# Kernel optimization log

Measured on AMD Instinct MI355X. Metric: run time of the kernel, lower is better.

Reference implementation:

```python
import jax, jax.numpy as jnp
import numpy as np

B, T, D, H = 4, 2048, 1024, 16
HD = D // H  # 64


def setup_inputs() -> dict:
    key = jax.random.key(0)
    k1, k2, k3 = jax.random.split(key, 3)
    x = jax.random.normal(k1, (B, T, D), dtype=jnp.float32)
    # xavier-uniform-ish scaling for stability
    W_qkv = jax.random.normal(k2, (3 * D, D), dtype=jnp.float32) * (1.0 / np.sqrt(D))
    W_proj = jax.random.normal(k3, (D, D), dtype=jnp.float32) * (1.0 / np.sqrt(D))
    b_proj = jnp.zeros((D,), dtype=jnp.float32)
    return {"x": x, "W_qkv": W_qkv, "W_proj": W_proj, "b_proj": b_proj}


def reference(x, W_qkv, W_proj, b_proj):
    Bx, Tx, C = x.shape
    qkv = x @ W_qkv.T                      # [B,T,3C]
    q, k, v = jnp.split(qkv, 3, axis=-1)
    # [B,T,C] -> [B,H,T,hd]
    def heads(t):
        return t.reshape(Bx, Tx, H, HD).transpose(0, 2, 1, 3)
    q, k, v = heads(q), heads(k), heads(v)
    scale = 1.0 / np.sqrt(HD)
    scores = jnp.einsum('bhqd,bhkd->bhqk', q, k) * scale  # [B,H,T,T]
    causal = jnp.tril(jnp.ones((Tx, Tx), dtype=bool))
    scores = jnp.where(causal, scores, jnp.finfo(scores.dtype).min)
    attn = jax.nn.softmax(scores, axis=-1)
    out = jnp.einsum('bhqk,bhkd->bhqd', attn, v)          # [B,H,T,hd]
    out = out.transpose(0, 2, 1, 3).reshape(Bx, Tx, C)    # [B,T,C]
    return out @ W_proj.T + b_proj
```

## Files before the change

kernel.cpp:

```cpp
#include <hip/hip_runtime.h>
#include <hip/hip_bf16.h>

#define B_  4
#define T_  2048
#define D_  1024
#define H_  16
#define HD_ 64
#define THREE_D (3 * D_)

typedef short s16x8 __attribute__((ext_vector_type(8)));
typedef float f32x4 __attribute__((ext_vector_type(4)));
typedef unsigned short u16;
typedef unsigned short u16x4 __attribute__((ext_vector_type(4)));

static __device__ __forceinline__ s16x8 load8(const u16* p) {
    return *reinterpret_cast<const s16x8*>(p);
}
static __device__ __forceinline__ u16 f2bf(float f) {
    __hip_bfloat16 h = __float2bfloat16(f);
    return *reinterpret_cast<u16*>(&h);
}
static __device__ __forceinline__ u16 bftrunc(float f) {
    unsigned u; __builtin_memcpy(&u, &f, 4); return (u16)(u >> 16);
}

static __device__ __forceinline__ void gload_lds16(const u16* g, u16* l) {
#if __has_builtin(__builtin_amdgcn_global_load_lds)
    __builtin_amdgcn_global_load_lds(
        (__attribute__((address_space(1))) void*)g,
        (__attribute__((address_space(3))) void*)l, 16, 0, 0);
#else
    *reinterpret_cast<s16x8*>(l) = load8(g);
#endif
}

__global__ __launch_bounds__(256) void cvt_f32_bf16(
    const float* __restrict__ in, u16* __restrict__ out, int n)
{
    const int i = (blockIdx.x * 256 + threadIdx.x) * 4;
    if (i < n) {
        const float4 f = *reinterpret_cast<const float4*>(in + i);
        u16x4 r;
        r.x = f2bf(f.x); r.y = f2bf(f.y); r.z = f2bf(f.z); r.w = f2bf(f.w);
        *reinterpret_cast<u16x4*>(out + i) = r;
    }
}

template<bool OUT_BF16>
__global__ __launch_bounds__(256) void gemm_bt128(
    const u16* __restrict__ A,
    const u16* __restrict__ Bm,
    void* __restrict__ Cv,
    const float* __restrict__ bias,
    int M, int N, int K, int lda, int ldb, int ldc,
    int qcols, float qsc)
{
    const int ntiles = N >> 7;
    const int mt = blockIdx.x / ntiles;
    const int nt = blockIdx.x % ntiles;
    const int m0 = mt * 128, n0 = nt * 128;
    const int tid  = threadIdx.x;
    const int lane = tid & 63;
    const int l15  = lane & 15;
    const int quad = lane >> 4;
    const int wave = tid >> 6;
    const int wm = (wave >> 1) * 64;
    const int wn = (wave & 1) * 64;

    __shared__ u16 A_sh[2][128 * 32];
    __shared__ u16 B_sh[2][128 * 32];

    f32x4 acc[4][4] = {};

    const int c0 = tid, c1 = tid + 256;
    const int ar0 = c0 >> 2, as0 = (c0 & 3) * 8;
    const int ar1 = c1 >> 2, as1 = (c1 & 3) * 8;
    const u16* Ag0 = A  + (size_t)(m0 + ar0) * lda + as0;
    const u16* Ag1 = A  + (size_t)(m0 + ar1) * lda + as1;
    const u16* Bg0 = Bm + (size_t)(n0 + ar0) * ldb + as0;
    const u16* Bg1 = Bm + (size_t)(n0 + ar1) * ldb + as1;

    for (int k0 = 0; k0 < K; k0 += 64) {
        __syncthreads();
        #pragma unroll
        for (int p = 0; p < 2; ++p) {
            gload_lds16(Ag0 + k0 + p * 32, &A_sh[p][c0 * 8]);
            gload_lds16(Ag1 + k0 + p * 32, &A_sh[p][c1 * 8]);
            gload_lds16(Bg0 + k0 + p * 32, &B_sh[p][c0 * 8]);
            gload_lds16(Bg1 + k0 + p * 32, &B_sh[p][c1 * 8]);
        }
        __syncthreads();

        #pragma unroll
        for (int p = 0; p < 2; ++p) {
            s16x8 a[4], b[4];
            #pragma unroll
            for (int i = 0; i < 4; ++i) {
                a[i] = *reinterpret_cast<const s16x8*>(&A_sh[p][(wm + i * 16 + l15) * 32 + quad * 8]);
                b[i] = *reinterpret_cast<const s16x8*>(&B_sh[p][(wn + i * 16 + l15) * 32 + quad * 8]);
            }
            #pragma unroll
            for (int mi = 0; mi < 4; ++mi)
                #pragma unroll
                for (int ni = 0; ni < 4; ++ni)
                    acc[mi][ni] = __builtin_amdgcn_mfma_f32_16x16x32_bf16(
                        a[mi], b[ni], acc[mi][ni], 0, 0, 0);
        }
    }

    #pragma unroll
    for (int ni = 0; ni < 4; ++ni) {
        const int col = n0 + wn + ni * 16 + l15;
        const float bv = bias ? bias[col] : 0.0f;
        const float sc = (col < qcols) ? qsc : 1.0f;
        #pragma unroll
        for (int mi = 0; mi < 4; ++mi) {
            const int row = m0 + wm + mi * 16 + quad * 4;
            #pragma unroll
            for (int r = 0; r < 4; ++r) {
                if (OUT_BF16)
                    ((u16*)Cv)[(size_t)(row + r) * ldc + col] = f2bf(acc[mi][ni][r] * sc + bv);
                else
                    ((float*)Cv)[(size_t)(row + r) * ldc + col] = acc[mi][ni][r] * sc + bv;
            }
        }
    }
}

__global__ __launch_bounds__(256) void transpose_v(
    const u16* __restrict__ qkv, u16* __restrict__ vt)
{
    const int nt = T_ / 64;
    const int tt = blockIdx.x % nt;
    const int bh = blockIdx.x / nt;
    const int t0 = tt * 64;
    __shared__ u16 tileT[64 * 72];
    const int tid = threadIdx.x;

    #pragma unroll
    for (int it = 0; it < 2; ++it) {
        const int c = tid + it * 256;
        const int t = c >> 3, fsub = c & 7;
        const s16x8 v = load8(qkv + (size_t)((bh >> 4) * T_ + t0 + t) * THREE_D
                                  + 2 * D_ + (bh & 15) * HD_ + fsub * 8);
        #pragma unroll
        for (int j = 0; j < 8; ++j)
            tileT[(fsub * 8 + j) * 72 + (t ^ (fsub << 3))] = (u16)v[j];
    }
    __syncthreads();
    #pragma unroll
    for (int it = 0; it < 2; ++it) {
        const int c = tid + it * 256;
        const int f = c >> 3, sub = c & 7;
        const s16x8 v = *reinterpret_cast<const s16x8*>(
            &tileT[f * 72 + ((sub ^ ((f >> 3) & 7)) << 3)]);
        *reinterpret_cast<s16x8*>(vt + (size_t)(bh * HD_ + f) * T_ + t0 + sub * 8) = v;
    }
}

__global__ __launch_bounds__(256) void flash_attn5(
    const u16* __restrict__ qkv, const u16* __restrict__ vt,
    u16* __restrict__ out)
{
    const int cls = blockIdx.x >> 6;
    const int bh  = blockIdx.x & 63;
    const int qmap[16] = {15,14,13,12, 8,9,10,11, 7,6,5,4, 0,1,2,3};
    const int qt = qmap[cls];
    const int h = bh & 15, b = bh >> 4;
    const int q0 = qt * 128;

    __shared__ u16 K_lds[64 * 72];
    __shared__ u16 V_lds[64 * 72];
    __shared__ u16 P_lds[4 * 32 * 72];

    const int tid = threadIdx.x;
    const int wave = tid >> 6, lane = tid & 63;
    const int l15 = lane & 15, quad = lane >> 4;
    u16* Pw = P_lds + wave * (32 * 72);

    const int w0 = q0 + wave * 32;

    s16x8 qf[2][2];
    #pragma unroll
    for (int mi = 0; mi < 2; ++mi) {
        const size_t rowQ = (size_t)(b * T_ + w0 + mi * 16 + l15) * THREE_D + h * HD_;
        qf[mi][0] = load8(qkv + rowQ + quad * 8);
        qf[mi][1] = load8(qkv + rowQ + 32 + quad * 8);
    }

    f32x4 o[2][4] = {};
    f32x4 osum[2] = {};

    s16x8 ones;
    #pragma unroll
    for (int j = 0; j < 8; ++j) ones[j] = (short)0x3F80;

    const int r0 = tid >> 3;
    const int s0 = (tid & 7) * 8;
    const u16* Kg0 = qkv + (size_t)(b * T_ + r0)      * THREE_D + D_ + h * HD_ + s0;
    const u16* Kg1 = qkv + (size_t)(b * T_ + r0 + 32) * THREE_D + D_ + h * HD_ + s0;
    const u16* Vg0 = vt + (size_t)(bh * HD_ + r0)      * T_ + s0;
    const u16* Vg1 = vt + (size_t)(bh * HD_ + r0 + 32) * T_ + s0;

    s16x8 pk0 = load8(Kg0);
    s16x8 pk1 = load8(Kg1);
    s16x8 pv0 = load8(Vg0);
    s16x8 pv1 = load8(Vg1);

    const int nkt = 2 * qt + 2;
    for (int kt = 0; kt < nkt; ++kt) {
        const int kbase = kt * 64;
        __syncthreads();
        *reinterpret_cast<s16x8*>(&K_lds[r0 * 72 + s0])        = pk0;
        *reinterpret_cast<s16x8*>(&K_lds[(r0 + 32) * 72 + s0]) = pk1;
        *reinterpret_cast<s16x8*>(&V_lds[r0 * 72 + s0])        = pv0;
        *reinterpret_cast<s16x8*>(&V_lds[(r0 + 32) * 72 + s0]) = pv1;
        __syncthreads();

        if (kt + 1 < nkt) {
            const int nb = kbase + 64;
            pk0 = load8(Kg0 + (size_t)nb * THREE_D);
            pk1 = load8(Kg1 + (size_t)nb * THREE_D);
            pv0 = load8(Vg0 + nb);
            pv1 = load8(Vg1 + nb);
        }

        if (kbase <= w0 + 31) {
            f32x4 s[2][4];
            #pragma unroll
            for (int n = 0; n < 4; ++n) {
                const s16x8 kf0 = *reinterpret_cast<const s16x8*>(
                    &K_lds[(n * 16 + l15) * 72 + quad * 8]);
                const s16x8 kf1 = *reinterpret_cast<const s16x8*>(
                    &K_lds[(n * 16 + l15) * 72 + 32 + quad * 8]);
                #pragma unroll
                for (int mi = 0; mi < 2; ++mi) {
                    f32x4 t = {};
                    t = __builtin_amdgcn_mfma_f32_16x16x32_bf16(qf[mi][0], kf0, t, 0, 0, 0);
                    t = __builtin_amdgcn_mfma_f32_16x16x32_bf16(qf[mi][1], kf1, t, 0, 0, 0);
                    s[mi][n] = t;
                }
            }

            if (kbase + 63 > w0) {
                #pragma unroll
                for (int mi = 0; mi < 2; ++mi)
                    #pragma unroll
                    for (int r = 0; r < 4; ++r) {
                        const int qr = w0 + mi * 16 + quad * 4 + r;
                        #pragma unroll
                        for (int n = 0; n < 4; ++n) {
                            const u16 p = (kbase + n * 16 + l15 > qr)
                                        ? (u16)0 : bftrunc(exp2f(s[mi][n][r]));
                            Pw[(mi * 16 + quad * 4 + r) * 72 + n * 16 + l15] = p;
                        }
                    }
            } else {
                #pragma unroll
                for (int mi = 0; mi < 2; ++mi)
                    #pragma unroll
                    for (int r = 0; r < 4; ++r)
                        #pragma unroll
                        for (int n = 0; n < 4; ++n)
                            Pw[(mi * 16 + quad * 4 + r) * 72 + n * 16 + l15] =
                                bftrunc(exp2f(s[mi][n][r]));
            }

            #pragma unroll
            for (int ks = 0; ks < 2; ++ks) {
                s16x8 pa[2];
                #pragma unroll
                for (int mi = 0; mi < 2; ++mi) {
                    pa[mi] = *reinterpret_cast<const s16x8*>(
                        &Pw[(mi * 16 + l15) * 72 + ks * 32 + quad * 8]);
                    osum[mi] = __builtin_amdgcn_mfma_f32_16x16x32_bf16(
                        pa[mi], ones, osum[mi], 0, 0, 0);
                }
                #pragma unroll
                for (int n4 = 0; n4 < 4; ++n4) {
                    const s16x8 vb = *reinterpret_cast<const s16x8*>(
                        &V_lds[(n4 * 16 + l15) * 72 + ks * 32 + quad * 8]);
                    #pragma unroll
                    for (int mi = 0; mi < 2; ++mi)
                        o[mi][n4] = __builtin_amdgcn_mfma_f32_16x16x32_bf16(
                            pa[mi], vb, o[mi][n4], 0, 0, 0);
                }
            }
        }
    }

    #pragma unroll
    for (int mi = 0; mi < 2; ++mi)
        #pragma unroll
        for (int r = 0; r < 4; ++r) {
            const float inv = 1.0f / osum[mi][r];
            const size_t rowO = (size_t)(b * T_ + w0 + mi * 16 + quad * 4 + r) * D_ + h * HD_;
            #pragma unroll
            for (int n4 = 0; n4 < 4; ++n4)
                out[rowO + n4 * 16 + l15] = f2bf(o[mi][n4][r] * inv);
        }
}

extern "C" void kernel_launch(void* const* d_in, const int* in_sizes, int n_in,
                              void* d_out, int out_size, void* d_ws, size_t ws_size,
                              hipStream_t stream)
{
    const float* x     = (const float*)d_in[0];
    const float* Wqkv  = (const float*)d_in[1];
    const float* Wproj = (const float*)d_in[2];
    const float* bproj = (const float*)d_in[3];
    float* out = (float*)d_out;

    const int M = B_ * T_;
    const float cs = 0.18033688011f;

    u16* xb    = (u16*)d_ws;
    u16* wqkvb = xb    + (size_t)M * D_;
    u16* wprob = wqkvb + (size_t)THREE_D * D_;
    u16* qkv   = wprob + (size_t)D_ * D_;
    u16* attn  = qkv   + (size_t)M * THREE_D;
    u16* vtb   = xb;

    {
        int n;
        n = M * D_;
        cvt_f32_bf16<<<dim3((n / 4 + 255) / 256), 256, 0, stream>>>(x, xb, n);
        n = THREE_D * D_;
        cvt_f32_bf16<<<dim3((n / 4 + 255) / 256), 256, 0, stream>>>(Wqkv, wqkvb, n);
        n = D_ * D_;
        cvt_f32_bf16<<<dim3((n / 4 + 255) / 256), 256, 0, stream>>>(Wproj, wprob, n);
    }

    gemm_bt128<true><<<dim3((M / 128) * (THREE_D / 128)), 256, 0, stream>>>(
        xb, wqkvb, qkv, nullptr, M, THREE_D, D_, D_, D_, THREE_D, D_, cs);

    transpose_v<<<dim3(B_ * H_ * (T_ / 64)), 256, 0, stream>>>(qkv, vtb);

    flash_attn5<<<dim3(B_ * H_ * (T_ / 128)), 256, 0, stream>>>(qkv, vtb, attn);

    gemm_bt128<false><<<dim3((M / 128) * (D_ / 128)), 256, 0, stream>>>(
        attn, wprob, out, bproj, M, D_, D_, D_, D_, D_, 0, 1.0f);
}
```

Before: 277.6 us.

## Fuse V transpose into QKV GEMM epilogue and vectorize P stores via swapped MFMA

The QKV GEMM epilogue now writes Q and K into a compact [M,2D] buffer and writes V straight into the transposed [B,H,HD,T] layout with 4-wide packed stores, so the separate transpose_v kernel and its round trip through memory go away. The attention kernel swaps the MFMA operand order so each lane holds 4 consecutive key scores for one query row. The P tile can then be written to LDS as packed u16x4 stores instead of scalar stores, and the causal masking is unified into one loop. The trade-off is scattered 8-byte global writes for V in the GEMM epilogue.

```diff
diff --git a/kernel.cpp b/kernel.cpp
--- a/kernel.cpp
+++ b/kernel.cpp
@@ -7,6 +7,7 @@
 #define H_  16
 #define HD_ 64
 #define THREE_D (3 * D_)
+#define TWO_D   (2 * D_)
 
 typedef short s16x8 __attribute__((ext_vector_type(8)));
 typedef float f32x4 __attribute__((ext_vector_type(4)));
@@ -46,14 +47,14 @@
     }
 }
 
-template<bool OUT_BF16>
+template<int MODE>
 __global__ __launch_bounds__(256) void gemm_bt128(
     const u16* __restrict__ A,
     const u16* __restrict__ Bm,
     void* __restrict__ Cv,
     const float* __restrict__ bias,
     int M, int N, int K, int lda, int ldb, int ldc,
-    int qcols, float qsc)
+    float qsc, u16* __restrict__ vt)
 {
     const int ntiles = N >> 7;
     const int mt = blockIdx.x / ntiles;
@@ -111,55 +112,44 @@
     #pragma unroll
     for (int ni = 0; ni < 4; ++ni) {
         const int col = n0 + wn + ni * 16 + l15;
-        const float bv = bias ? bias[col] : 0.0f;
-        const float sc = (col < qcols) ? qsc : 1.0f;
-        #pragma unroll
-        for (int mi = 0; mi < 4; ++mi) {
-            const int row = m0 + wm + mi * 16 + quad * 4;
-            #pragma unroll
-            for (int r = 0; r < 4; ++r) {
-                if (OUT_BF16)
-                    ((u16*)Cv)[(size_t)(row + r) * ldc + col] = f2bf(acc[mi][ni][r] * sc + bv);
-                else
-                    ((float*)Cv)[(size_t)(row + r) * ldc + col] = acc[mi][ni][r] * sc + bv;
-            }
-        }
-    }
-}
-
-__global__ __launch_bounds__(256) void transpose_v(
-    const u16* __restrict__ qkv, u16* __restrict__ vt)
-{
-    const int nt = T_ / 64;
-    const int tt = blockIdx.x % nt;
-    const int bh = blockIdx.x / nt;
-    const int t0 = tt * 64;
-    __shared__ u16 tileT[64 * 72];
-    const int tid = threadIdx.x;
-
-    #pragma unroll
-    for (int it = 0; it < 2; ++it) {
-        const int c = tid + it * 256;
-        const int t = c >> 3, fsub = c & 7;
-        const s16x8 v = load8(qkv + (size_t)((bh >> 4) * T_ + t0 + t) * THREE_D
-                                  + 2 * D_ + (bh & 15) * HD_ + fsub * 8);
-        #pragma unroll
-        for (int j = 0; j < 8; ++j)
-            tileT[(fsub * 8 + j) * 72 + (t ^ (fsub << 3))] = (u16)v[j];
-    }
-    __syncthreads();
-    #pragma unroll
-    for (int it = 0; it < 2; ++it) {
-        const int c = tid + it * 256;
-        const int f = c >> 3, sub = c & 7;
-        const s16x8 v = *reinterpret_cast<const s16x8*>(
-            &tileT[f * 72 + ((sub ^ ((f >> 3) & 7)) << 3)]);
-        *reinterpret_cast<s16x8*>(vt + (size_t)(bh * HD_ + f) * T_ + t0 + sub * 8) = v;
-    }
-}
-
-__global__ __launch_bounds__(256) void flash_attn5(
-    const u16* __restrict__ qkv, const u16* __restrict__ vt,
+        if (MODE == 0) {
+            const float bv = bias ? bias[col] : 0.0f;
+            #pragma unroll
+            for (int mi = 0; mi < 4; ++mi) {
+                const int row = m0 + wm + mi * 16 + quad * 4;
+                #pragma unroll
+                for (int r = 0; r < 4; ++r)
+                    ((float*)Cv)[(size_t)(row + r) * ldc + col] = acc[mi][ni][r] + bv;
+            }
+        } else {
+            if (col < TWO_D) {
+                const float sc = (col < D_) ? qsc : 1.0f;
+                #pragma unroll
+                for (int mi = 0; mi < 4; ++mi) {
+                    const int row = m0 + wm + mi * 16 + quad * 4;
+                    #pragma unroll
+                    for (int r = 0; r < 4; ++r)
+                        ((u16*)Cv)[(size_t)(row + r) * ldc + col] = f2bf(acc[mi][ni][r] * sc);
+                }
+            } else {
+                const int vc = col - TWO_D;
+                #pragma unroll
+                for (int mi = 0; mi < 4; ++mi) {
+                    const int row = m0 + wm + mi * 16 + quad * 4;
+                    const int bb = row >> 11, t = row & (T_ - 1);
+                    u16x4 pk;
+                    #pragma unroll
+                    for (int r = 0; r < 4; ++r) pk[r] = f2bf(acc[mi][ni][r]);
+                    *reinterpret_cast<u16x4*>(
+                        vt + ((size_t)(bb * H_ * HD_) + vc) * T_ + t) = pk;
+                }
+            }
+        }
+    }
+}
+
+__global__ __launch_bounds__(256) void flash_attn6(
+    const u16* __restrict__ qk, const u16* __restrict__ vt,
     u16* __restrict__ out)
 {
     const int cls = blockIdx.x >> 6;
@@ -183,9 +173,9 @@
     s16x8 qf[2][2];
     #pragma unroll
     for (int mi = 0; mi < 2; ++mi) {
-        const size_t rowQ = (size_t)(b * T_ + w0 + mi * 16 + l15) * THREE_D + h * HD_;
-        qf[mi][0] = load8(qkv + rowQ + quad * 8);
-        qf[mi][1] = load8(qkv + rowQ + 32 + quad * 8);
+        const size_t rowQ = (size_t)(b * T_ + w0 + mi * 16 + l15) * TWO_D + h * HD_;
+        qf[mi][0] = load8(qk + rowQ + quad * 8);
+        qf[mi][1] = load8(qk + rowQ + 32 + quad * 8);
     }
 
     f32x4 o[2][4] = {};
@@ -197,8 +187,8 @@
 
     const int r0 = tid >> 3;
     const int s0 = (tid & 7) * 8;
-    const u16* Kg0 = qkv + (size_t)(b * T_ + r0)      * THREE_D + D_ + h * HD_ + s0;
-    const u16* Kg1 = qkv + (size_t)(b * T_ + r0 + 32) * THREE_D + D_ + h * HD_ + s0;
+    const u16* Kg0 = qk + (size_t)(b * T_ + r0)      * TWO_D + D_ + h * HD_ + s0;
+    const u16* Kg1 = qk + (size_t)(b * T_ + r0 + 32) * TWO_D + D_ + h * HD_ + s0;
     const u16* Vg0 = vt + (size_t)(bh * HD_ + r0)      * T_ + s0;
     const u16* Vg1 = vt + (size_t)(bh * HD_ + r0 + 32) * T_ + s0;
 
@@ -219,14 +209,14 @@
 
         if (kt + 1 < nkt) {
             const int nb = kbase + 64;
-            pk0 = load8(Kg0 + (size_t)nb * THREE_D);
-            pk1 = load8(Kg1 + (size_t)nb * THREE_D);
+            pk0 = load8(Kg0 + (size_t)nb * TWO_D);
+            pk1 = load8(Kg1 + (size_t)nb * TWO_D);
             pv0 = load8(Vg0 + nb);
             pv1 = load8(Vg1 + nb);
         }
 
         if (kbase <= w0 + 31) {
-            f32x4 s[2][4];
+            f32x4 st[2][4];
             #pragma unroll
             for (int n = 0; n < 4; ++n) {
                 const s16x8 kf0 = *reinterpret_cast<const s16x8*>(
@@ -236,34 +226,31 @@
                 #pragma unroll
                 for (int mi = 0; mi < 2; ++mi) {
                     f32x4 t = {};
-                    t = __builtin_amdgcn_mfma_f32_16x16x32_bf16(qf[mi][0], kf0, t, 0, 0, 0);
-                    t = __builtin_amdgcn_mfma_f32_16x16x32_bf16(qf[mi][1], kf1, t, 0, 0, 0);
-                    s[mi][n] = t;
-                }
-            }
-
-            if (kbase + 63 > w0) {
-                #pragma unroll
-                for (int mi = 0; mi < 2; ++mi)
-                    #pragma unroll
-                    for (int r = 0; r < 4; ++r) {
-                        const int qr = w0 + mi * 16 + quad * 4 + r;
-                        #pragma unroll
-                        for (int n = 0; n < 4; ++n) {
-                            const u16 p = (kbase + n * 16 + l15 > qr)
-                                        ? (u16)0 : bftrunc(exp2f(s[mi][n][r]));
-                            Pw[(mi * 16 + quad * 4 + r) * 72 + n * 16 + l15] = p;
-                        }
-                    }
-            } else {
-                #pragma unroll
-                for (int mi = 0; mi < 2; ++mi)
+                    t = __builtin_amdgcn_mfma_f32_16x16x32_bf16(kf0, qf[mi][0], t, 0, 0, 0);
+                    t = __builtin_amdgcn_mfma_f32_16x16x32_bf16(kf1, qf[mi][1], t, 0, 0, 0);
+                    st[mi][n] = t;
+                }
+            }
+
+            const bool diag = (kbase + 63 > w0);
+            #pragma unroll
+            for (int mi = 0; mi < 2; ++mi) {
+                const int qr = w0 + mi * 16 + l15;
+                #pragma unroll
+                for (int n = 0; n < 4; ++n) {
+                    const int kb = kbase + n * 16 + quad * 4;
+                    u16x4 pk;
                     #pragma unroll
                     for (int r = 0; r < 4; ++r)
+                        pk[r] = bftrunc(exp2f(st[mi][n][r]));
+                    if (diag) {
                         #pragma unroll
-                        for (int n = 0; n < 4; ++n)
-                            Pw[(mi * 16 + quad * 4 + r) * 72 + n * 16 + l15] =
-                                bftrunc(exp2f(s[mi][n][r]));
+                        for (int r = 0; r < 4; ++r)
+                            if (kb + r > qr) pk[r] = 0;
+                    }
+                    *reinterpret_cast<u16x4*>(
+                        &Pw[(mi * 16 + l15) * 72 + n * 16 + quad * 4]) = pk;
+                }
             }
 
             #pragma unroll
@@ -317,9 +304,9 @@
     u16* xb    = (u16*)d_ws;
     u16* wqkvb = xb    + (size_t)M * D_;
     u16* wprob = wqkvb + (size_t)THREE_D * D_;
-    u16* qkv   = wprob + (size_t)D_ * D_;
-    u16* attn  = qkv   + (size_t)M * THREE_D;
-    u16* vtb   = xb;
+    u16* qk    = wprob + (size_t)D_ * D_;
+    u16* vtb   = qk    + (size_t)M * TWO_D;
+    u16* attn  = vtb   + (size_t)B_ * H_ * HD_ * T_;
 
     {
         int n;
@@ -331,13 +318,11 @@
         cvt_f32_bf16<<<dim3((n / 4 + 255) / 256), 256, 0, stream>>>(Wproj, wprob, n);
     }
 
-    gemm_bt128<true><<<dim3((M / 128) * (THREE_D / 128)), 256, 0, stream>>>(
-        xb, wqkvb, qkv, nullptr, M, THREE_D, D_, D_, D_, THREE_D, D_, cs);
-
-    transpose_v<<<dim3(B_ * H_ * (T_ / 64)), 256, 0, stream>>>(qkv, vtb);
-
-    flash_attn5<<<dim3(B_ * H_ * (T_ / 128)), 256, 0, stream>>>(qkv, vtb, attn);
-
-    gemm_bt128<false><<<dim3((M / 128) * (D_ / 128)), 256, 0, stream>>>(
-        attn, wprob, out, bproj, M, D_, D_, D_, D_, D_, 0, 1.0f);
-}
+    gemm_bt128<1><<<dim3((M / 128) * (THREE_D / 128)), 256, 0, stream>>>(
+        xb, wqkvb, qk, nullptr, M, THREE_D, D_, D_, D_, TWO_D, cs, vtb);
+
+    flash_attn6<<<dim3(B_ * H_ * (T_ / 128)), 256, 0, stream>>>(qk, vtb, attn);
+
+    gemm_bt128<0><<<dim3((M / 128) * (D_ / 128)), 256, 0, stream>>>(
+        attn, wprob, out, bproj, M, D_, D_, D_, D_, D_, 1.0f, nullptr);
+}
```

Measured after the change: 256.8 us. 1.08x faster.
